# Optimization experiments

Hardware: AMD Instinct MI355X
Metric: run time of the kernel (lower is better)

## Reference

```python
import jax, jax.numpy as jnp
import numpy as np

N, D, R, O = 4096, 128, 256, 64


def setup_inputs() -> dict:
    key = jax.random.key(0)
    k1, k2, k3, k4 = jax.random.split(key, 4)
    X = jax.random.normal(k1, (N, D), dtype=jnp.float32)
    # Gaussian membership params per rule: centers and (positive) widths, shape [R, D]
    centers = 0.5 * jax.random.normal(k2, (R, D), dtype=jnp.float32)
    sigmas = 1.5 + jax.random.uniform(k3, (R, D), dtype=jnp.float32)  # in [1.5, 2.5]
    # Takagi-Sugeno per-rule linear coeffs [R, D+1, O] (last row = bias)
    coeffs = 0.02 * jax.random.normal(k4, (R, D + 1, O), dtype=jnp.float32)
    return {"X": X, "centers": centers, "sigmas": sigmas, "coeffs": coeffs}


def reference(X, centers, sigmas, coeffs):
    # Layer 1: Gaussian memberships for all rules at once: [N, R, D]
    diff = X[:, None, :] - centers[None, :, :]
    memb = jnp.exp(-(diff * diff) / (2.0 * sigmas * sigmas)[None, :, :])
    # Layer 2: rule strengths via product over input dims ('prod' strategy): [N, R]
    strengths = jnp.prod(memb, axis=2)
    # Layer 3: normalize across rules
    norm = strengths / (jnp.sum(strengths, axis=1, keepdims=True) + 1e-8)
    # Layer 4: per-rule linear consequents: [N, R, O]
    weighted = jnp.einsum('ni,rij->nrj', X, coeffs[:, :-1, :]) + coeffs[:, -1, :][None, :, :]
    # Layer 5: weighted combine over rules: [N, O]
    out = jnp.einsum('nr,nrj->nj', norm, weighted)
    # task='classification' -> Softmax(dim=1)
    return jax.nn.softmax(out, axis=1)
```

## Files before the change

kernel.cpp:

```cpp
#include <hip/hip_runtime.h>

#define N_SAMPLES 4096
#define D_IN      128
#define R_RULES   256
#define O_OUT     64
#define KPAD      136
#define NCHUNK    17
#define CH_I      8
#define NGROUPS   8

typedef _Float16 f16;
typedef _Float16 f16x2 __attribute__((ext_vector_type(2)));
typedef _Float16 f16x4 __attribute__((ext_vector_type(4)));
typedef _Float16 f16x8 __attribute__((ext_vector_type(8)));
typedef float    f32x4 __attribute__((ext_vector_type(4)));

__global__ __launch_bounds__(128) void anfis_prep2(
    const float* __restrict__ centers, const float* __restrict__ sigmas,
    f16* __restrict__ Bext) {
  const int r = blockIdx.x;
  const int d = threadIdx.x;
  const float c = centers[(size_t)r * 128 + d];
  const float s = sigmas[(size_t)r * 128 + d];
  const float iv = 0.5f / (s * s);
  const float b1 = -iv;
  const float b2 = 2.0f * c * iv;
  f16 b1h = (f16)b1; f16 b1l = (f16)(b1 - (float)b1h);
  f16 b2h = (f16)b2; f16 b2l = (f16)(b2 - (float)b2h);
  auto put = [&](int k, f16 v) {
    Bext[((size_t)(k >> 3) * 256 + r) * 8 + (k & 7)] = v;
  };
  put(d, b1h);
  put(128 + d, b1l);
  put(256 + d, b1h);
  put(384 + d, b2h);
  put(512 + d, b2l);
  put(640 + d, b2h);
  float p = -c * c * iv;
#pragma unroll
  for (int off = 32; off; off >>= 1) p += __shfl_xor(p, off, 64);
  __shared__ float red[2];
  if ((threadIdx.x & 63) == 0) red[threadIdx.x >> 6] = p;
  __syncthreads();
  if (d < 30) put(770 + d, (f16)0.0f);
  if (d == 0) {
    float k2 = red[0] + red[1];
    f16 h = (f16)k2; f16 l = (f16)(k2 - (float)h);
    put(768, h);
    put(769, l);
  }
}

__global__ __launch_bounds__(512) void anfis_s16(
    const float* __restrict__ X, const f16* __restrict__ Bext,
    float* __restrict__ S) {
  __shared__ alignas(16) f16 Xq[32 * 512];
  const int tid = threadIdx.x;
  const int m0 = (blockIdx.x >> 1) * 32;
  const int r0 = (blockIdx.x & 1) * 128;
  const int w = tid >> 6, lane = tid & 63;
  const int mg = w >> 2, ng = w & 3;
  const int lm = lane & 15, quad = lane >> 4;

  {
    int m = tid >> 4, oct = tid & 15;
    const float* src = X + (size_t)(m0 + m) * 128 + oct * 8;
    float4 a = reinterpret_cast<const float4*>(src)[0];
    float4 b = reinterpret_cast<const float4*>(src)[1];
    float xs[8] = {a.x, a.y, a.z, a.w, b.x, b.y, b.z, b.w};
    f16x8 vh, vl, v2h, v2l;
#pragma unroll
    for (int q = 0; q < 8; ++q) {
      float x = xs[q];
      f16 h = (f16)x;   f16 l = (f16)(x - (float)h);
      float x2 = x * x;
      f16 h2 = (f16)x2; f16 l2 = (f16)(x2 - (float)h2);
      vh[q] = h; vl[q] = l; v2h[q] = h2; v2l[q] = l2;
    }
    f16x8* row = reinterpret_cast<f16x8*>(&Xq[m * 512]);
    int sw = m & 7;
    row[(0 * 16 + oct) ^ sw] = v2h;
    row[(1 * 16 + oct) ^ sw] = v2l;
    row[(2 * 16 + oct) ^ sw] = vh;
    row[(3 * 16 + oct) ^ sw] = vl;
  }
  __syncthreads();

  f32x4 acc[2] = {};
  const int am = mg * 16 + lm;
  const f16x8* arow = reinterpret_cast<const f16x8*>(&Xq[am * 512]);
  const int asw = am & 7;
  const int col0 = r0 + ng * 32 + lm;

#pragma unroll
  for (int t = 0; t < 24; ++t) {
    const int seg = t >> 2;
    const int plane = (seg < 2) ? 0 : (seg == 2) ? 1 : (seg < 5) ? 2 : 3;
    const int o = t * 4 + quad;
    f16x8 av = arow[(plane * 16 + (o & 15)) ^ asw];
    const f16* bp = Bext + ((size_t)o * 256 + col0) * 8;
    f16x8 b0 = *reinterpret_cast<const f16x8*>(bp);
    f16x8 b1 = *reinterpret_cast<const f16x8*>(bp + 16 * 8);
    acc[0] = __builtin_amdgcn_mfma_f32_16x16x32_f16(av, b0, acc[0], 0, 0, 0);
    acc[1] = __builtin_amdgcn_mfma_f32_16x16x32_f16(av, b1, acc[1], 0, 0, 0);
  }
  {
    f16x8 av = {};
    if (quad == 0) { av[0] = (f16)1.0f; av[1] = (f16)1.0f; }
    const int o = 96 + quad;
    const f16* bp = Bext + ((size_t)o * 256 + col0) * 8;
    f16x8 b0 = *reinterpret_cast<const f16x8*>(bp);
    f16x8 b1 = *reinterpret_cast<const f16x8*>(bp + 16 * 8);
    acc[0] = __builtin_amdgcn_mfma_f32_16x16x32_f16(av, b0, acc[0], 0, 0, 0);
    acc[1] = __builtin_amdgcn_mfma_f32_16x16x32_f16(av, b1, acc[1], 0, 0, 0);
  }
#pragma unroll
  for (int nf = 0; nf < 2; ++nf)
#pragma unroll
    for (int q = 0; q < 4; ++q) {
      int row = m0 + mg * 16 + quad * 4 + q;
      int col = r0 + ng * 32 + nf * 16 + lm;
      S[(size_t)row * R_RULES + col] = __expf(acc[nf][q]);
    }
}

__global__ __launch_bounds__(256) void anfis_den(
    const float* __restrict__ S, float* __restrict__ invden) {
  const int n = blockIdx.x * 4 + (threadIdx.x >> 6);
  const int lane = threadIdx.x & 63;
  float4 v = reinterpret_cast<const float4*>(S)[(size_t)n * 64 + lane];
  float s = (v.x + v.y) + (v.z + v.w);
#pragma unroll
  for (int off = 32; off; off >>= 1) s += __shfl_xor(s, off, 64);
  if (lane == 0) invden[n] = 1.0f / (s + 1e-8f);
}

__global__ __launch_bounds__(256) void anfis_prep(
    const float* __restrict__ coeffs, f16* __restrict__ Cp) {
  __shared__ alignas(16) f16 T[64 * 32];
  const int i = blockIdx.x;
  const int g = blockIdx.y;
  const int tid = threadIdx.x;
  const int rg = tid & 31;
  const int jb = tid >> 5;
  if (i < 129) {
    const float* src = coeffs + ((size_t)(g * 32 + rg) * 129 + i) * 64 + jb * 8;
    float4 a = reinterpret_cast<const float4*>(src)[0];
    float4 b = reinterpret_cast<const float4*>(src)[1];
    T[(jb * 8 + 0) * 32 + rg] = (f16)a.x;
    T[(jb * 8 + 1) * 32 + rg] = (f16)a.y;
    T[(jb * 8 + 2) * 32 + rg] = (f16)a.z;
    T[(jb * 8 + 3) * 32 + rg] = (f16)a.w;
    T[(jb * 8 + 4) * 32 + rg] = (f16)b.x;
    T[(jb * 8 + 5) * 32 + rg] = (f16)b.y;
    T[(jb * 8 + 6) * 32 + rg] = (f16)b.z;
    T[(jb * 8 + 7) * 32 + rg] = (f16)b.w;
  } else {
#pragma unroll
    for (int q = 0; q < 8; ++q) T[(jb * 8 + q) * 32 + rg] = (f16)0.0f;
  }
  __syncthreads();
  f16x8* dst = reinterpret_cast<f16x8*>(
      Cp + (((size_t)g * NCHUNK + (i >> 3)) * CH_I + (i & 7)) * 2048);
  dst[tid] = reinterpret_cast<const f16x8*>(T)[tid];
}

__global__ __launch_bounds__(256) void anfis_main16(
    const float* __restrict__ X, const float* __restrict__ S,
    const float* __restrict__ invden, const f16* __restrict__ Cp,
    float* __restrict__ part) {
  __shared__ alignas(16) f16 Xs[64 * KPAD];
  const int tid = threadIdx.x;
  const int g = blockIdx.x & 7;
  const int m0 = (blockIdx.x >> 3) * 64;
  const int w = tid >> 6, lane = tid & 63;
  const int mg = w >> 1, ng = w & 1;
  const int lm = lane & 15, quad = lane >> 4;

#pragma unroll
  for (int it = 0; it < 8; ++it) {
    int fi = tid + (it << 8);
    int m = fi >> 5, k4 = (fi & 31) << 2;
    float4 v = reinterpret_cast<const float4*>(X)[(size_t)(m0 + m) * 32 + (fi & 31)];
    f16x4 h = {(f16)v.x, (f16)v.y, (f16)v.z, (f16)v.w};
    *reinterpret_cast<f16x4*>(&Xs[m * KPAD + k4]) = h;
  }
  if (tid < 64) {
    f16x8 bias = {};
    bias[0] = (f16)1.0f;
    *reinterpret_cast<f16x8*>(&Xs[tid * KPAD + 128]) = bias;
  }

  union F8 { f16x8 v; f16x2 h[4]; };
  F8 pf[2];
#pragma unroll
  for (int mf = 0; mf < 2; ++mf) {
    int row = m0 + mg * 32 + mf * 16 + lm;
    const float invd = invden[row];
    const float* pp = S + (size_t)row * R_RULES + g * 32 + quad * 8;
    float4 p0 = reinterpret_cast<const float4*>(pp)[0];
    float4 p1 = reinterpret_cast<const float4*>(pp)[1];
    pf[mf].h[0] = f16x2{(f16)(p0.x * invd), (f16)(p0.y * invd)};
    pf[mf].h[1] = f16x2{(f16)(p0.z * invd), (f16)(p0.w * invd)};
    pf[mf].h[2] = f16x2{(f16)(p1.x * invd), (f16)(p1.y * invd)};
    pf[mf].h[3] = f16x2{(f16)(p1.z * invd), (f16)(p1.w * invd)};
  }
  __syncthreads();

  f32x4 acc[2][2] = {};
  const f16* bpl = Cp + (size_t)g * NCHUNK * CH_I * 2048
                 + ((ng * 32 + lm) * 32 + quad * 8);

  for (int c = 0; c < NCHUNK; ++c) {
    f16x8 xv[2];
    xv[0] = *reinterpret_cast<const f16x8*>(&Xs[(mg * 32 + lm) * KPAD + c * 8]);
    xv[1] = *reinterpret_cast<const f16x8*>(&Xs[(mg * 32 + 16 + lm) * KPAD + c * 8]);
    const f16* bpc = bpl + (size_t)c * (CH_I * 2048);
#pragma unroll
    for (int ii = 0; ii < CH_I; ++ii) {
      f16x8 b0 = *reinterpret_cast<const f16x8*>(bpc + ii * 2048);
      f16x8 b1 = *reinterpret_cast<const f16x8*>(bpc + ii * 2048 + 512);
      F8 a[2];
#pragma unroll
      for (int mf = 0; mf < 2; ++mf) {
        f16 xvv = xv[mf][ii];
        f16x2 xd = {xvv, xvv};
        a[mf].h[0] = pf[mf].h[0] * xd;
        a[mf].h[1] = pf[mf].h[1] * xd;
        a[mf].h[2] = pf[mf].h[2] * xd;
        a[mf].h[3] = pf[mf].h[3] * xd;
      }
      acc[0][0] = __builtin_amdgcn_mfma_f32_16x16x32_f16(a[0].v, b0, acc[0][0], 0, 0, 0);
      acc[0][1] = __builtin_amdgcn_mfma_f32_16x16x32_f16(a[0].v, b1, acc[0][1], 0, 0, 0);
      acc[1][0] = __builtin_amdgcn_mfma_f32_16x16x32_f16(a[1].v, b0, acc[1][0], 0, 0, 0);
      acc[1][1] = __builtin_amdgcn_mfma_f32_16x16x32_f16(a[1].v, b1, acc[1][1], 0, 0, 0);
    }
  }

#pragma unroll
  for (int mf = 0; mf < 2; ++mf)
#pragma unroll
    for (int nf = 0; nf < 2; ++nf)
#pragma unroll
      for (int q = 0; q < 4; ++q) {
        int row = m0 + mg * 32 + mf * 16 + quad * 4 + q;
        int col = ng * 32 + nf * 16 + lm;
        part[((size_t)g * N_SAMPLES + row) * O_OUT + col] = acc[mf][nf][q];
      }
}

__global__ __launch_bounds__(256) void anfis_out(
    const float* __restrict__ part, float* __restrict__ out) {
  const int n = blockIdx.x * 4 + (threadIdx.x >> 6);
  const int lane = threadIdx.x & 63;
  const size_t stride = (size_t)N_SAMPLES * O_OUT;
  const float* p0 = part + (size_t)n * O_OUT + lane;
  float v = 0.f;
#pragma unroll
  for (int gg = 0; gg < 8; ++gg) v += p0[gg * stride];
  float mx = v;
#pragma unroll
  for (int off = 32; off; off >>= 1) mx = fmaxf(mx, __shfl_xor(mx, off, 64));
  float e = __expf(v - mx);
  float s = e;
#pragma unroll
  for (int off = 32; off; off >>= 1) s += __shfl_xor(s, off, 64);
  out[(size_t)n * O_OUT + lane] = e / s;
}

extern "C" void kernel_launch(void* const* d_in, const int* in_sizes, int n_in,
                              void* d_out, int out_size, void* d_ws, size_t ws_size,
                              hipStream_t stream) {
  const float* X       = (const float*)d_in[0];
  const float* centers = (const float*)d_in[1];
  const float* sigmas  = (const float*)d_in[2];
  const float* coeffs  = (const float*)d_in[3];
  float* out = (float*)d_out;

  float* S    = (float*)d_ws;
  float* part = S + (size_t)N_SAMPLES * R_RULES;
  f16*   Cp   = (f16*)(part + (size_t)NGROUPS * N_SAMPLES * O_OUT);
  f16*   Bext = Cp + (size_t)NGROUPS * NCHUNK * CH_I * 2048;
  float* invden = (float*)(Bext + (size_t)100 * 256 * 8);

  anfis_prep2<<<R_RULES, 128, 0, stream>>>(centers, sigmas, Bext);
  anfis_prep<<<dim3(KPAD, NGROUPS), 256, 0, stream>>>(coeffs, Cp);
  anfis_s16<<<256, 512, 0, stream>>>(X, Bext, S);
  anfis_den<<<N_SAMPLES / 4, 256, 0, stream>>>(S, invden);
  anfis_main16<<<512, 256, 0, stream>>>(X, S, invden, Cp, part);
  anfis_out<<<N_SAMPLES / 4, 256, 0, stream>>>(part, out);
}
```

Before: 121.6 us.

## Stage coefficient tiles into LDS via global_load_lds and repartition waves by output column

The main kernel now copies each chunk of four input-dim coefficient slices into shared memory with direct global-to-LDS loads, replacing per-wave global fragment reads. The wave split is rebuilt so each wave owns 16 output columns across all 64 rows, which means four accumulators and four probability fragments per wave. Launch bounds now request 4 blocks per SM. This aims to cut redundant global traffic for the coefficients, but it adds two barriers per chunk and doubles the chunk count with no double buffering, so load latency is exposed.

```diff
diff --git a/kernel.cpp b/kernel.cpp
--- a/kernel.cpp
+++ b/kernel.cpp
@@ -7,6 +7,8 @@
 #define KPAD      136
 #define NCHUNK    17
 #define CH_I      8
+#define CH4       4
+#define NCH4      34
 #define NGROUPS   8
 
 typedef _Float16 f16;
@@ -165,16 +167,16 @@
   dst[tid] = reinterpret_cast<const f16x8*>(T)[tid];
 }
 
-__global__ __launch_bounds__(256) void anfis_main16(
+__global__ __launch_bounds__(256, 4) void anfis_main16(
     const float* __restrict__ X, const float* __restrict__ S,
     const float* __restrict__ invden, const f16* __restrict__ Cp,
     float* __restrict__ part) {
   __shared__ alignas(16) f16 Xs[64 * KPAD];
+  __shared__ alignas(16) f16 Bs[CH4 * 64 * 32];
   const int tid = threadIdx.x;
   const int g = blockIdx.x & 7;
   const int m0 = (blockIdx.x >> 3) * 64;
   const int w = tid >> 6, lane = tid & 63;
-  const int mg = w >> 1, ng = w & 1;
   const int lm = lane & 15, quad = lane >> 4;
 
 #pragma unroll
@@ -192,10 +194,10 @@
   }
 
   union F8 { f16x8 v; f16x2 h[4]; };
-  F8 pf[2];
-#pragma unroll
-  for (int mf = 0; mf < 2; ++mf) {
-    int row = m0 + mg * 32 + mf * 16 + lm;
+  F8 pf[4];
+#pragma unroll
+  for (int mf = 0; mf < 4; ++mf) {
+    int row = m0 + mf * 16 + lm;
     const float invd = invden[row];
     const float* pp = S + (size_t)row * R_RULES + g * 32 + quad * 8;
     float4 p0 = reinterpret_cast<const float4*>(pp)[0];
@@ -205,48 +207,52 @@
     pf[mf].h[2] = f16x2{(f16)(p1.x * invd), (f16)(p1.y * invd)};
     pf[mf].h[3] = f16x2{(f16)(p1.z * invd), (f16)(p1.w * invd)};
   }
-  __syncthreads();
-
-  f32x4 acc[2][2] = {};
-  const f16* bpl = Cp + (size_t)g * NCHUNK * CH_I * 2048
-                 + ((ng * 32 + lm) * 32 + quad * 8);
-
-  for (int c = 0; c < NCHUNK; ++c) {
-    f16x8 xv[2];
-    xv[0] = *reinterpret_cast<const f16x8*>(&Xs[(mg * 32 + lm) * KPAD + c * 8]);
-    xv[1] = *reinterpret_cast<const f16x8*>(&Xs[(mg * 32 + 16 + lm) * KPAD + c * 8]);
-    const f16* bpc = bpl + (size_t)c * (CH_I * 2048);
-#pragma unroll
-    for (int ii = 0; ii < CH_I; ++ii) {
-      f16x8 b0 = *reinterpret_cast<const f16x8*>(bpc + ii * 2048);
-      f16x8 b1 = *reinterpret_cast<const f16x8*>(bpc + ii * 2048 + 512);
-      F8 a[2];
-#pragma unroll
-      for (int mf = 0; mf < 2; ++mf) {
+
+  f32x4 acc[4] = {};
+  const char* cpg = (const char*)Cp + (size_t)g * KPAD * 4096;
+
+  for (int c = 0; c < NCH4; ++c) {
+    __syncthreads();
+    const char* gsrc = cpg + (size_t)c * 16384;
+#pragma unroll
+    for (int it = 0; it < 4; ++it) {
+      int off = (it << 12) + (w << 10);
+      __builtin_amdgcn_global_load_lds(
+          (const __attribute__((address_space(1))) unsigned int*)(gsrc + off + lane * 16),
+          (__attribute__((address_space(3))) unsigned int*)((char*)Bs + off),
+          16, 0, 0);
+    }
+    __syncthreads();
+    f16x4 xv[4];
+#pragma unroll
+    for (int mf = 0; mf < 4; ++mf)
+      xv[mf] = *reinterpret_cast<const f16x4*>(&Xs[(mf * 16 + lm) * KPAD + c * 4]);
+#pragma unroll
+    for (int ii = 0; ii < CH4; ++ii) {
+      f16x8 b = *reinterpret_cast<const f16x8*>(
+          &Bs[(ii * 64 + w * 16 + lm) * 32 + quad * 8]);
+#pragma unroll
+      for (int mf = 0; mf < 4; ++mf) {
         f16 xvv = xv[mf][ii];
         f16x2 xd = {xvv, xvv};
-        a[mf].h[0] = pf[mf].h[0] * xd;
-        a[mf].h[1] = pf[mf].h[1] * xd;
-        a[mf].h[2] = pf[mf].h[2] * xd;
-        a[mf].h[3] = pf[mf].h[3] * xd;
+        F8 a;
+        a.h[0] = pf[mf].h[0] * xd;
+        a.h[1] = pf[mf].h[1] * xd;
+        a.h[2] = pf[mf].h[2] * xd;
+        a.h[3] = pf[mf].h[3] * xd;
+        acc[mf] = __builtin_amdgcn_mfma_f32_16x16x32_f16(a.v, b, acc[mf], 0, 0, 0);
       }
-      acc[0][0] = __builtin_amdgcn_mfma_f32_16x16x32_f16(a[0].v, b0, acc[0][0], 0, 0, 0);
-      acc[0][1] = __builtin_amdgcn_mfma_f32_16x16x32_f16(a[0].v, b1, acc[0][1], 0, 0, 0);
-      acc[1][0] = __builtin_amdgcn_mfma_f32_16x16x32_f16(a[1].v, b0, acc[1][0], 0, 0, 0);
-      acc[1][1] = __builtin_amdgcn_mfma_f32_16x16x32_f16(a[1].v, b1, acc[1][1], 0, 0, 0);
-    }
-  }
-
-#pragma unroll
-  for (int mf = 0; mf < 2; ++mf)
-#pragma unroll
-    for (int nf = 0; nf < 2; ++nf)
-#pragma unroll
-      for (int q = 0; q < 4; ++q) {
-        int row = m0 + mg * 32 + mf * 16 + quad * 4 + q;
-        int col = ng * 32 + nf * 16 + lm;
-        part[((size_t)g * N_SAMPLES + row) * O_OUT + col] = acc[mf][nf][q];
-      }
+    }
+  }
+
+#pragma unroll
+  for (int mf = 0; mf < 4; ++mf)
+#pragma unroll
+    for (int q = 0; q < 4; ++q) {
+      int row = m0 + mf * 16 + quad * 4 + q;
+      int col = w * 16 + lm;
+      part[((size_t)g * N_SAMPLES + row) * O_OUT + col] = acc[mf][q];
+    }
 }
 
 __global__ __launch_bounds__(256) void anfis_out(
```

Result: faster. 115.1 us (-5.4%).
